# Kernel tuning notes

Measured on AMD Instinct MI355X. Metric: run time of the kernel, lower is better.

The kernel has to match this reference:

```python
import jax, jax.numpy as jnp
import numpy as np

B, T, M, P = 1024, 128, 256, 256  # batch, timesteps, encoder_hidden, decoder_hidden
Tm1 = T - 1


def setup_inputs() -> dict:
    key = jax.random.key(0)
    ks = jax.random.split(key, 10)
    s = lambda k, shape: jax.random.normal(k, shape, jnp.float32) * 0.05
    return {
        "X_encoded": jax.random.normal(ks[0], (B, Tm1, M), jnp.float32),
        "y_prev": jax.random.normal(ks[1], (B, Tm1), jnp.float32),
        # attn_layer: Linear(2P+M -> M), Tanh, Linear(M -> 1)
        "attn_W1": s(ks[2], (M, 2 * P + M)),
        "attn_b1": jnp.zeros((M,), jnp.float32),
        "attn_W2": s(ks[3], (1, M)),
        "attn_b2": jnp.zeros((1,), jnp.float32),
        # LSTM(input_size=1, hidden=P), gate order i,f,g,o
        "W_ih": s(ks[4], (4 * P, 1)),
        "W_hh": s(ks[5], (4 * P, P)),
        "b_ih": jnp.zeros((4 * P,), jnp.float32),
        "b_hh": jnp.zeros((4 * P,), jnp.float32),
        # fc: Linear(M+1 -> 1) (weights init'd normal_() in torch)
        "fc_W": jax.random.normal(ks[6], (1, M + 1), jnp.float32),
        "fc_b": jnp.zeros((1,), jnp.float32),
        # fc_final: Linear(P+M -> 1)
        "fcf_W": s(ks[7], (1, P + M)),
        "fcf_b": jnp.zeros((1,), jnp.float32),
    }


def reference(X_encoded, y_prev, attn_W1, attn_b1, attn_W2, attn_b2,
              W_ih, W_hh, b_ih, b_hh, fc_W, fc_b, fcf_W, fcf_b):
    Bsz, Tsteps, Mdim = X_encoded.shape
    Pdim = W_hh.shape[1]

    def step(carry, y_t):
        d, c, _ = carry  # d,c: [B,P]
        dm = jnp.broadcast_to(d[:, None, :], (Bsz, Tsteps, Pdim))
        cm = jnp.broadcast_to(c[:, None, :], (Bsz, Tsteps, Pdim))
        x = jnp.concatenate([dm, cm, X_encoded], axis=2)  # [B,T-1,2P+M]
        e = jnp.tanh(jnp.einsum('bti,hi->bth', x, attn_W1) + attn_b1)
        scores = jnp.einsum('bth,oh->bto', e, attn_W2)[..., 0] + attn_b2[0]  # [B,T-1]
        beta = jax.nn.softmax(scores, axis=-1)
        context = jnp.einsum('bt,btm->bm', beta, X_encoded)  # [B,M]
        y_tilde = jnp.concatenate([context, y_t[:, None]], axis=1) @ fc_W.T + fc_b  # [B,1]
        gates = y_tilde @ W_ih.T + d @ W_hh.T + (b_ih + b_hh)  # [B,4P]
        i, f, g, o = jnp.split(gates, 4, axis=1)
        c_new = jax.nn.sigmoid(f) * c + jax.nn.sigmoid(i) * jnp.tanh(g)
        d_new = jax.nn.sigmoid(o) * jnp.tanh(c_new)
        return (d_new, c_new, context), None

    init = (jnp.zeros((Bsz, Pdim), X_encoded.dtype),
            jnp.zeros((Bsz, Pdim), X_encoded.dtype),
            jnp.zeros((Bsz, Mdim), X_encoded.dtype))
    (d, c, context), _ = jax.lax.scan(step, init, y_prev.T)  # scan over T-1 steps
    y_pred = jnp.concatenate([d, context], axis=1) @ fcf_W.T + fcf_b  # [B,1]
    return y_pred
```

## Files before the change

kernel.cpp:

```cpp
#include <hip/hip_runtime.h>
#include <hip/hip_bf16.h>

#define TT 127
#define L2E 1.4426950408889634f

typedef __attribute__((ext_vector_type(8))) short s8v;
typedef __attribute__((ext_vector_type(4))) float f4v;

__device__ __forceinline__ float bf2f(unsigned short u){
  union { unsigned int i; float f; } v; v.i = ((unsigned int)u) << 16; return v.f;
}
__device__ __forceinline__ unsigned short f2bf(float f){
  union { float f; unsigned int i; } v; v.f = f;
  unsigned int r = v.i + 0x7FFFu + ((v.i >> 16) & 1u);
  return (unsigned short)(r >> 16);
}
__device__ __forceinline__ float fexp2(float x){ return __builtin_amdgcn_exp2f(x); }
__device__ __forceinline__ float frcp(float x){ return __builtin_amdgcn_rcpf(x); }
__device__ __forceinline__ float sigm(float x){
  return frcp(1.f + fexp2(-L2E * x));
}
__device__ __forceinline__ float tanh_f(float x){
  return 1.f - 2.f * frcp(1.f + fexp2(2.f * L2E * x));
}
__device__ __forceinline__ f4v mfma16(s8v a, s8v b, f4v c){
  return __builtin_amdgcn_mfma_f32_16x16x32_bf16(a, b, c, 0, 0, 0);
}
__device__ __forceinline__ void barrier_lgkm(){
  asm volatile("s_waitcnt lgkmcnt(0)" ::: "memory");
  __builtin_amdgcn_s_barrier();
}

__global__ void k_pack_w1dc(const float* __restrict__ W1, unsigned short* __restrict__ WP){
  int n = blockIdx.x * 256 + threadIdx.x;
  int lane = n & 63, w = (n >> 6) & 15, kt = n >> 10;
  int h = w * 16 + (lane & 15);
  int i0 = kt * 32 + (lane >> 4) * 8;
  #pragma unroll
  for (int j = 0; j < 8; ++j)
    WP[(size_t)n * 8 + j] = f2bf(W1[h * 768 + i0 + j]);
}
__global__ void k_pack_whh(const float* __restrict__ Whh, unsigned short* __restrict__ WP){
  int n = blockIdx.x * 256 + threadIdx.x;
  int lane = n & 63, w = (n >> 6) & 15, f = n >> 10;
  int ct = f >> 3, kt = f & 7;
  int g = (w * 4 + ct) * 16 + (lane & 15);
  int i0 = kt * 32 + (lane >> 4) * 8;
  #pragma unroll
  for (int j = 0; j < 8; ++j)
    WP[131072 + (size_t)n * 8 + j] = f2bf(Whh[g * 256 + i0 + j]);
}

__global__ void k_tr_w1x(const float* __restrict__ W1, float* __restrict__ W1xT){
  int idx = blockIdx.x * 256 + threadIdx.x;
  int k = idx >> 8, h = idx & 255;
  W1xT[idx] = W1[h * 768 + 512 + k];
}

__global__ void k_xfg(const float* __restrict__ X, const float* __restrict__ fcW,
                      const float* __restrict__ fcfW,
                      float* __restrict__ xf, float* __restrict__ xg){
  const int b = blockIdx.x;
  const int w = threadIdx.x >> 6, lane = threadIdx.x & 63;
  f4v wf = *(const f4v*)&fcW[lane * 4];
  f4v wg = *(const f4v*)&fcfW[256 + lane * 4];
  for (int t = w; t < TT; t += 4) {
    f4v x = *(const f4v*)&X[((size_t)b * TT + t) * 256 + lane * 4];
    float af = x[0]*wf[0] + x[1]*wf[1] + x[2]*wf[2] + x[3]*wf[3];
    float ag = x[0]*wg[0] + x[1]*wg[1] + x[2]*wg[2] + x[3]*wg[3];
    #pragma unroll
    for (int m = 32; m; m >>= 1) { af += __shfl_xor(af, m); ag += __shfl_xor(ag, m); }
    if (lane == 0) { xf[(size_t)b * TT + t] = af; xg[(size_t)b * TT + t] = ag; }
  }
}

__global__ __launch_bounds__(256) void k_gemm_tx(
    const float* __restrict__ X, const float* __restrict__ W1xT,
    const float* __restrict__ b1, unsigned short* __restrict__ Tx)
{
  __shared__ float As[16][64];
  __shared__ float Bs[16][64];
  const int row0 = blockIdx.x * 64;
  const int col0 = blockIdx.y * 64;
  const int tid = threadIdx.x;
  const int tx = tid & 15, ty = tid >> 4;
  float acc[4][4] = {};
  for (int k0 = 0; k0 < 256; k0 += 16) {
    {
      const int rr = tid & 63, kk4 = (tid >> 6) << 2;
      float4 v = *(const float4*)&X[(size_t)(row0 + rr) * 256 + k0 + kk4];
      As[kk4 + 0][rr] = v.x; As[kk4 + 1][rr] = v.y;
      As[kk4 + 2][rr] = v.z; As[kk4 + 3][rr] = v.w;
    }
    {
      const int cc = tid & 63, kb = tid >> 6;
      #pragma unroll
      for (int j = 0; j < 4; ++j)
        Bs[kb + 4 * j][cc] = W1xT[(size_t)(k0 + kb + 4 * j) * 256 + col0 + cc];
    }
    __syncthreads();
    #pragma unroll
    for (int kk = 0; kk < 16; ++kk) {
      float4 a4 = *(const float4*)&As[kk][ty << 2];
      float4 b4 = *(const float4*)&Bs[kk][tx << 2];
      float av[4] = {a4.x, a4.y, a4.z, a4.w};
      float bv[4] = {b4.x, b4.y, b4.z, b4.w};
      #pragma unroll
      for (int i = 0; i < 4; ++i)
        #pragma unroll
        for (int j = 0; j < 4; ++j)
          acc[i][j] = fmaf(av[i], bv[j], acc[i][j]);
    }
    __syncthreads();
  }
  const int c = col0 + (tx << 2);
  #pragma unroll
  for (int i = 0; i < 4; ++i) {
    const int r = row0 + (ty << 2) + i;
    ushort4 o;
    o.x = f2bf(tanhf(acc[i][0] + b1[c + 0]));
    o.y = f2bf(tanhf(acc[i][1] + b1[c + 1]));
    o.z = f2bf(tanhf(acc[i][2] + b1[c + 2]));
    o.w = f2bf(tanhf(acc[i][3] + b1[c + 3]));
    *(ushort4*)&Tx[(size_t)r * 256 + c] = o;
  }
}

__global__ __launch_bounds__(1024, 4) void k_main(
    const unsigned short* __restrict__ Tx,
    const unsigned short* __restrict__ WP,
    const float* __restrict__ xf,
    const float* __restrict__ xg,
    const float* __restrict__ yprev,
    const float* __restrict__ W2,
    const float* __restrict__ Wih,
    const float* __restrict__ bih,
    const float* __restrict__ bhh,
    const float* __restrict__ fcW,
    const float* __restrict__ fcb,
    const float* __restrict__ fcfW,
    const float* __restrict__ fcfb,
    float* __restrict__ out)
{
  __shared__ __align__(16) char wring[6 * 16384];
  __shared__ __align__(16) unsigned short dcA[16][520];
  __shared__ __align__(16) float us_s[4][320];
  __shared__ __align__(16) float sc[4][128];
  __shared__ __align__(16) float gts[4][1024];
  __shared__ float w2s[256];
  __shared__ float fcfw_s[256];
  __shared__ float wih_s[1024];
  __shared__ float bsum_s[1024];
  __shared__ float yp_s[4][128];
  __shared__ float xf_s[4][128];
  __shared__ float xg_s[4][128];
  __shared__ float ytil[4];
  __shared__ float sg_s[4];

  const int tid = threadIdx.x;
  const int lane = tid & 63;
  const int w = tid >> 6;
  const int bb = tid >> 8;
  const int hq = tid & 255;
  const int b0 = blockIdx.x << 2;
  const int bq = w >> 2;
  const int cc = lane & 15;
  const int g4 = lane >> 4;

  if (tid < 256) w2s[tid] = W2[tid];
  if (tid >= 256 && tid < 512) fcfw_s[tid - 256] = fcfW[tid - 256];
  wih_s[tid] = Wih[tid];
  bsum_s[tid] = bih[tid] + bhh[tid];
  if (tid < 512 && (tid & 127) < TT)
    yp_s[tid >> 7][tid & 127] = yprev[(size_t)(b0 + (tid >> 7)) * TT + (tid & 127)];
  if (tid >= 512) {
    const int r = (tid - 512) >> 7, c = tid & 127;
    float vf = 0.f, vg = 0.f;
    if (c < TT) {
      vf = xf[(size_t)(b0 + r) * TT + c];
      vg = xg[(size_t)(b0 + r) * TT + c];
    }
    xf_s[r][c] = vf;
    xg_s[r][c] = vg;
  }
  for (int i = tid; i < 16 * 520; i += 1024)
    (&dcA[0][0])[i] = 0;
  const float fcw256 = fcW[256];
  const float fcb0 = fcb[0];
  const float fcfb0 = fcfb[0];
  float creg = 0.f, dreg = 0.f;
  barrier_lgkm();

  const int arow = lane & 15;
  const char* dcbase = (const char*)&dcA[0][0] + arow * 1040 + ((lane >> 4) << 4);
  const int wlo = w * 1024 + lane * 16;
  const char* WPc = (const char*)WP;
  const char* wslice = wring + wlo;
  char* wdst = wring + w * 1024;

  #pragma unroll
  for (int F = 0; F < 6; ++F) {
    __builtin_amdgcn_global_load_lds((const unsigned int*)(WPc + (size_t)F * 16384 + wlo),
                                     (unsigned int*)(wdst + F * 16384), 16, 0, 0);
  }
  asm volatile("s_waitcnt vmcnt(5)" ::: "memory");
  __builtin_amdgcn_sched_barrier(0);
  s8v bnext = *(const s8v*)(wslice);

  for (int t = 0; t < TT; ++t) {
    {
      f4v au0 = {0.f,0.f,0.f,0.f}, au1 = au0;
      f4v ag0 = au0, ag1 = au0, ag2 = au0, ag3 = au0;
      #pragma unroll
      for (int f = 0; f < 48; ++f) {
        s8v bcur = bnext;
        asm volatile("s_waitcnt vmcnt(4)" ::: "memory");
        __builtin_amdgcn_sched_barrier(0);
        bnext = *(const s8v*)(wslice + (((f + 1) % 6) * 16384));
        const int kt = (f < 16) ? f : (f & 7);
        s8v av = *(const s8v*)(dcbase + kt * 64);
        if (f < 16) {
          if (f & 1) au1 = mfma16(av, bcur, au1);
          else       au0 = mfma16(av, bcur, au0);
        } else if (f < 24) {
          ag0 = mfma16(av, bcur, ag0);
        } else if (f < 32) {
          ag1 = mfma16(av, bcur, ag1);
        } else if (f < 40) {
          ag2 = mfma16(av, bcur, ag2);
        } else {
          ag3 = mfma16(av, bcur, ag3);
        }
        const int nf = (f + 6) % 48;
        __builtin_amdgcn_global_load_lds((const unsigned int*)(WPc + (size_t)nf * 16384 + wlo),
                                         (unsigned int*)(wdst + (f % 6) * 16384), 16, 0, 0);
      }
      f4v au = au0 + au1;
      #pragma unroll
      for (int r = 0; r < 4; ++r) {
        au[r] += __shfl_xor(au[r], 16);
        ag0[r] += __shfl_xor(ag0[r], 16);
        ag1[r] += __shfl_xor(ag1[r], 16);
        ag2[r] += __shfl_xor(ag2[r], 16);
        ag3[r] += __shfl_xor(ag3[r], 16);
      }
      if (lane < 16) {
        const int hp = w * 20 + lane;
        #pragma unroll
        for (int r = 0; r < 4; ++r)
          us_s[r][hp] = tanh_f(au[r]);
        #pragma unroll
        for (int r = 0; r < 4; ++r) {
          gts[r][(w * 4 + 0) * 16 + lane] = ag0[r];
          gts[r][(w * 4 + 1) * 16 + lane] = ag1[r];
          gts[r][(w * 4 + 2) * 16 + lane] = ag2[r];
          gts[r][(w * 4 + 3) * 16 + lane] = ag3[r];
        }
      }
    }
    barrier_lgkm();

    {
      float tur[16], w2r[16];
      #pragma unroll
      for (int e4 = 0; e4 < 4; ++e4) {
        f4v tv = *(const f4v*)&us_s[bq][cc * 20 + e4 * 4];
        f4v wv = *(const f4v*)&w2s[cc * 16 + e4 * 4];
        tur[e4*4+0] = tv[0]; tur[e4*4+1] = tv[1]; tur[e4*4+2] = tv[2]; tur[e4*4+3] = tv[3];
        w2r[e4*4+0] = wv[0]; w2r[e4*4+1] = wv[1]; w2r[e4*4+2] = wv[2]; w2r[e4*4+3] = wv[3];
      }
      const unsigned short* txb = &Tx[((size_t)(b0 + bq) * TT) * 256 + cc * 16];
      #pragma unroll
      for (int it = 0; it < 8; ++it) {
        const int tt = it * 16 + (w & 3) * 4 + g4;
        const int ttc = tt < 126 ? tt : 126;
        const unsigned short* p = txb + (size_t)ttc * 256;
        s8v xa = *(const s8v*)p;
        s8v xb = *(const s8v*)(p + 8);
        float a0 = 0.f, a1 = 0.f;
        #pragma unroll
        for (int e = 0; e < 8; ++e) {
          const float x = bf2f((unsigned short)xa[e]);
          a0 = fmaf(w2r[e] * (tur[e] + x), frcp(fmaf(tur[e], x, 1.f)), a0);
        }
        #pragma unroll
        for (int e = 0; e < 8; ++e) {
          const float x = bf2f((unsigned short)xb[e]);
          a1 = fmaf(w2r[8 + e] * (tur[8 + e] + x), frcp(fmaf(tur[8 + e], x, 1.f)), a1);
        }
        float acc = a0 + a1;
        acc += __shfl_xor(acc, 1);
        acc += __shfl_xor(acc, 2);
        acc += __shfl_xor(acc, 4);
        acc += __shfl_xor(acc, 8);
        if (cc == 0 && tt < TT) sc[bq][tt] = acc;
      }
    }
    barrier_lgkm();

    if (w < 4) {
      const float s0 = sc[w][lane];
      const float s1 = (lane < 63) ? sc[w][lane + 64] : -3.0e38f;
      float mx = fmaxf(s0, s1);
      #pragma unroll
      for (int m = 32; m; m >>= 1) mx = fmaxf(mx, __shfl_xor(mx, m));
      const float p0 = fexp2((s0 - mx) * L2E);
      const float p1 = (lane < 63) ? fexp2((s1 - mx) * L2E) : 0.f;
      float sm = p0 + p1;
      float af = fmaf(p0, xf_s[w][lane], p1 * xf_s[w][(lane + 64) & 127]);
      #pragma unroll
      for (int m = 32; m; m >>= 1) {
        sm += __shfl_xor(sm, m);
        af += __shfl_xor(af, m);
      }
      const float inv = frcp(sm);
      if (lane == 0)
        ytil[w] = af * inv + fcw256 * yp_s[w][t] + fcb0;
      if (t == TT - 1) {
        float ag_ = fmaf(p0, xg_s[w][lane], p1 * xg_s[w][(lane + 64) & 127]);
        #pragma unroll
        for (int m = 32; m; m >>= 1) ag_ += __shfl_xor(ag_, m);
        if (lane == 0) sg_s[w] = ag_ * inv;
      }
    }
    barrier_lgkm();

    {
      const float yt = ytil[bb];
      const float gi = gts[bb][hq]       + yt * wih_s[hq]       + bsum_s[hq];
      const float gf = gts[bb][hq + 256] + yt * wih_s[hq + 256] + bsum_s[hq + 256];
      const float gg = gts[bb][hq + 512] + yt * wih_s[hq + 512] + bsum_s[hq + 512];
      const float go = gts[bb][hq + 768] + yt * wih_s[hq + 768] + bsum_s[hq + 768];
      creg = sigm(gf) * creg + sigm(gi) * tanh_f(gg);
      dreg = sigm(go) * tanh_f(creg);
      const unsigned short dh = f2bf(dreg);
      const unsigned short dl = f2bf(dreg - bf2f(dh));
      const unsigned short ch = f2bf(creg);
      const unsigned short cl = f2bf(creg - bf2f(ch));
      dcA[bb][hq] = dh;           dcA[bb + 4][hq] = dl;
      dcA[bb][256 + hq] = ch;     dcA[bb + 4][256 + hq] = cl;
    }
    barrier_lgkm();
  }

  us_s[bb][hq] = dreg;
  barrier_lgkm();
  if (w < 4) {
    float a = 0.f;
    #pragma unroll
    for (int j = 0; j < 4; ++j) {
      const int m = lane + (j << 6);
      a = fmaf(us_s[w][m], fcfw_s[m], a);
    }
    #pragma unroll
    for (int m = 32; m; m >>= 1) a += __shfl_xor(a, m);
    if (lane == 0) out[b0 + w] = a + sg_s[w] + fcfb0;
  }
  asm volatile("s_waitcnt vmcnt(0)" ::: "memory");
}

extern "C" void kernel_launch(void* const* d_in, const int* in_sizes, int n_in,
                              void* d_out, int out_size, void* d_ws, size_t ws_size,
                              hipStream_t stream) {
  const float* X    = (const float*)d_in[0];
  const float* yprev= (const float*)d_in[1];
  const float* W1   = (const float*)d_in[2];
  const float* b1   = (const float*)d_in[3];
  const float* W2   = (const float*)d_in[4];
  const float* Wih  = (const float*)d_in[6];
  const float* Whh  = (const float*)d_in[7];
  const float* bih  = (const float*)d_in[8];
  const float* bhh  = (const float*)d_in[9];
  const float* fcW  = (const float*)d_in[10];
  const float* fcb  = (const float*)d_in[11];
  const float* fcfW = (const float*)d_in[12];
  const float* fcfb = (const float*)d_in[13];
  float* out = (float*)d_out;

  size_t off = 0;
  char* base = (char*)d_ws;
  auto alloc = [&](size_t bytes) -> void* {
    void* p = base + off;
    off += (bytes + 255) & ~(size_t)255;
    return p;
  };
  const size_t txBytes = (size_t)1024 * TT * 256 * 2;
  unsigned short* Tx   = (unsigned short*)alloc(txBytes);
  unsigned short* WP   = (unsigned short*)alloc((size_t)48 * 16384);
  float* W1xT          = (float*)alloc((size_t)256 * 256 * 4);
  float* xf            = (float*)alloc((size_t)1024 * TT * 4);
  float* xg            = (float*)alloc((size_t)1024 * TT * 4);
  (void)in_sizes; (void)n_in; (void)out_size; (void)ws_size;

  k_pack_w1dc<<<64, 256, 0, stream>>>(W1, WP);
  k_pack_whh<<<128, 256, 0, stream>>>(Whh, WP);
  k_tr_w1x<<<256, 256, 0, stream>>>(W1, W1xT);
  k_xfg<<<1024, 256, 0, stream>>>(X, fcW, fcfW, xf, xg);
  dim3 gg(2032, 4);
  k_gemm_tx<<<gg, 256, 0, stream>>>(X, W1xT, b1, Tx);
  k_main<<<256, 1024, 0, stream>>>(Tx, WP, xf, xg, yprev, W2,
                                   Wih, bih, bhh, fcW, fcb, fcfW, fcfb, out);
}
```

Baseline: 4.273 ms.

## Quantize precomputed tanh attention term to int8 and swizzle LDS hidden-state layout

Stores the precomputed tanh(X·W1x+b1) tensor as int8 scaled by 127 instead of bf16. This halves the global-memory traffic the main recurrent kernel re-reads every timestep, and the tanh-addition identity is rewritten to fold the scale into precomputed weights. It also changes the LDS layout of the d/c MFMA operand to an XOR-swizzled padded layout to reduce bank conflicts. The int8 quantization lowers the precision of the attention scores and may affect numerical tolerance.

```diff
diff --git a/kernel.cpp b/kernel.cpp
--- a/kernel.cpp
+++ b/kernel.cpp
@@ -6,6 +6,7 @@
 
 typedef __attribute__((ext_vector_type(8))) short s8v;
 typedef __attribute__((ext_vector_type(4))) float f4v;
+typedef __attribute__((ext_vector_type(4))) int i4v;
 
 __device__ __forceinline__ float bf2f(unsigned short u){
   union { unsigned int i; float f; } v; v.i = ((unsigned int)u) << 16; return v.f;
@@ -76,7 +77,7 @@
 
 __global__ __launch_bounds__(256) void k_gemm_tx(
     const float* __restrict__ X, const float* __restrict__ W1xT,
-    const float* __restrict__ b1, unsigned short* __restrict__ Tx)
+    const float* __restrict__ b1, char* __restrict__ Tx8)
 {
   __shared__ float As[16][64];
   __shared__ float Bs[16][64];
@@ -117,17 +118,17 @@
   #pragma unroll
   for (int i = 0; i < 4; ++i) {
     const int r = row0 + (ty << 2) + i;
-    ushort4 o;
-    o.x = f2bf(tanhf(acc[i][0] + b1[c + 0]));
-    o.y = f2bf(tanhf(acc[i][1] + b1[c + 1]));
-    o.z = f2bf(tanhf(acc[i][2] + b1[c + 2]));
-    o.w = f2bf(tanhf(acc[i][3] + b1[c + 3]));
-    *(ushort4*)&Tx[(size_t)r * 256 + c] = o;
+    uchar4 o;
+    o.x = (unsigned char)(char)rintf(tanhf(acc[i][0] + b1[c + 0]) * 127.f);
+    o.y = (unsigned char)(char)rintf(tanhf(acc[i][1] + b1[c + 1]) * 127.f);
+    o.z = (unsigned char)(char)rintf(tanhf(acc[i][2] + b1[c + 2]) * 127.f);
+    o.w = (unsigned char)(char)rintf(tanhf(acc[i][3] + b1[c + 3]) * 127.f);
+    *(uchar4*)&Tx8[(size_t)r * 256 + c] = o;
   }
 }
 
 __global__ __launch_bounds__(1024, 4) void k_main(
-    const unsigned short* __restrict__ Tx,
+    const char* __restrict__ Tx8,
     const unsigned short* __restrict__ WP,
     const float* __restrict__ xf,
     const float* __restrict__ xg,
@@ -143,7 +144,7 @@
     float* __restrict__ out)
 {
   __shared__ __align__(16) char wring[6 * 16384];
-  __shared__ __align__(16) unsigned short dcA[16][520];
+  __shared__ __align__(16) char dcA8[16 * 1152];
   __shared__ __align__(16) float us_s[4][320];
   __shared__ __align__(16) float sc[4][128];
   __shared__ __align__(16) float gts[4][1024];
@@ -183,8 +184,8 @@
     xf_s[r][c] = vf;
     xg_s[r][c] = vg;
   }
-  for (int i = tid; i < 16 * 520; i += 1024)
-    (&dcA[0][0])[i] = 0;
+  for (int i = tid; i < 16 * 1152 / 2; i += 1024)
+    ((unsigned short*)dcA8)[i] = 0;
   const float fcw256 = fcW[256];
   const float fcb0 = fcb[0];
   const float fcfb0 = fcfb[0];
@@ -192,7 +193,9 @@
   barrier_lgkm();
 
   const int arow = lane & 15;
-  const char* dcbase = (const char*)&dcA[0][0] + arow * 1040 + ((lane >> 4) << 4);
+  const char* arbase = dcA8 + arow * 1152;
+  const int sx4 = (arow & 7) << 4;
+  const int g16 = (lane >> 4) << 4;
   const int wlo = w * 1024 + lane * 16;
   const char* WPc = (const char*)WP;
   const char* wslice = wring + wlo;
@@ -218,7 +221,7 @@
         __builtin_amdgcn_sched_barrier(0);
         bnext = *(const s8v*)(wslice + (((f + 1) % 6) * 16384));
         const int kt = (f < 16) ? f : (f & 7);
-        s8v av = *(const s8v*)(dcbase + kt * 64);
+        s8v av = *(const s8v*)(arbase + ((kt * 64 + g16) ^ sx4));
         if (f < 16) {
           if (f & 1) au1 = mfma16(av, bcur, au1);
           else       au0 = mfma16(av, bcur, au0);
@@ -261,34 +264,38 @@
     barrier_lgkm();
 
     {
-      float tur[16], w2r[16];
+      float tur[16], w2r[16], wt127[16];
       #pragma unroll
       for (int e4 = 0; e4 < 4; ++e4) {
         f4v tv = *(const f4v*)&us_s[bq][cc * 20 + e4 * 4];
         f4v wv = *(const f4v*)&w2s[cc * 16 + e4 * 4];
-        tur[e4*4+0] = tv[0]; tur[e4*4+1] = tv[1]; tur[e4*4+2] = tv[2]; tur[e4*4+3] = tv[3];
-        w2r[e4*4+0] = wv[0]; w2r[e4*4+1] = wv[1]; w2r[e4*4+2] = wv[2]; w2r[e4*4+3] = wv[3];
-      }
-      const unsigned short* txb = &Tx[((size_t)(b0 + bq) * TT) * 256 + cc * 16];
+        #pragma unroll
+        for (int j = 0; j < 4; ++j) {
+          tur[e4*4+j] = tv[j];
+          w2r[e4*4+j] = wv[j];
+          wt127[e4*4+j] = wv[j] * tv[j] * 127.f;
+        }
+      }
+      const char* txb = &Tx8[((size_t)(b0 + bq) * TT) * 256 + cc * 16];
       #pragma unroll
       for (int it = 0; it < 8; ++it) {
         const int tt = it * 16 + (w & 3) * 4 + g4;
         const int ttc = tt < 126 ? tt : 126;
-        const unsigned short* p = txb + (size_t)ttc * 256;
-        s8v xa = *(const s8v*)p;
-        s8v xb = *(const s8v*)(p + 8);
-        float a0 = 0.f, a1 = 0.f;
-        #pragma unroll
-        for (int e = 0; e < 8; ++e) {
-          const float x = bf2f((unsigned short)xa[e]);
-          a0 = fmaf(w2r[e] * (tur[e] + x), frcp(fmaf(tur[e], x, 1.f)), a0);
+        i4v dv = *(const i4v*)(txb + (size_t)ttc * 256);
+        float acc = 0.f;
+        #pragma unroll
+        for (int j = 0; j < 4; ++j) {
+          const int d = dv[j];
+          const float x0 = (float)((d << 24) >> 24);
+          const float x1 = (float)((d << 16) >> 24);
+          const float x2 = (float)((d << 8) >> 24);
+          const float x3 = (float)(d >> 24);
+          const int e = j * 4;
+          acc = fmaf(fmaf(w2r[e+0], x0, wt127[e+0]), frcp(fmaf(tur[e+0], x0, 127.f)), acc);
+          acc = fmaf(fmaf(w2r[e+1], x1, wt127[e+1]), frcp(fmaf(tur[e+1], x1, 127.f)), acc);
+          acc = fmaf(fmaf(w2r[e+2], x2, wt127[e+2]), frcp(fmaf(tur[e+2], x2, 127.f)), acc);
+          acc = fmaf(fmaf(w2r[e+3], x3, wt127[e+3]), frcp(fmaf(tur[e+3], x3, 127.f)), acc);
         }
-        #pragma unroll
-        for (int e = 0; e < 8; ++e) {
-          const float x = bf2f((unsigned short)xb[e]);
-          a1 = fmaf(w2r[8 + e] * (tur[8 + e] + x), frcp(fmaf(tur[8 + e], x, 1.f)), a1);
-        }
-        float acc = a0 + a1;
         acc += __shfl_xor(acc, 1);
         acc += __shfl_xor(acc, 2);
         acc += __shfl_xor(acc, 4);
@@ -337,8 +344,14 @@
       const unsigned short dl = f2bf(dreg - bf2f(dh));
       const unsigned short ch = f2bf(creg);
       const unsigned short cl = f2bf(creg - bf2f(ch));
-      dcA[bb][hq] = dh;           dcA[bb + 4][hq] = dl;
-      dcA[bb][256 + hq] = ch;     dcA[bb + 4][256 + hq] = cl;
+      const int cd = 2 * hq;
+      const int ccol = 512 + 2 * hq;
+      const int sh = (bb & 7) << 4;
+      const int sl = ((bb + 4) & 7) << 4;
+      *(unsigned short*)(dcA8 + bb * 1152       + (((cd & ~15) ^ sh) | (cd & 15)))   = dh;
+      *(unsigned short*)(dcA8 + (bb + 4) * 1152 + (((cd & ~15) ^ sl) | (cd & 15)))   = dl;
+      *(unsigned short*)(dcA8 + bb * 1152       + (((ccol & ~15) ^ sh) | (ccol & 15))) = ch;
+      *(unsigned short*)(dcA8 + (bb + 4) * 1152 + (((ccol & ~15) ^ sl) | (ccol & 15))) = cl;
     }
     barrier_lgkm();
   }
@@ -384,8 +397,7 @@
     off += (bytes + 255) & ~(size_t)255;
     return p;
   };
-  const size_t txBytes = (size_t)1024 * TT * 256 * 2;
-  unsigned short* Tx   = (unsigned short*)alloc(txBytes);
+  char* Tx8            = (char*)alloc((size_t)1024 * TT * 256);
   unsigned short* WP   = (unsigned short*)alloc((size_t)48 * 16384);
   float* W1xT          = (float*)alloc((size_t)256 * 256 * 4);
   float* xf            = (float*)alloc((size_t)1024 * TT * 4);
@@ -397,7 +409,7 @@
   k_tr_w1x<<<256, 256, 0, stream>>>(W1, W1xT);
   k_xfg<<<1024, 256, 0, stream>>>(X, fcW, fcfW, xf, xg);
   dim3 gg(2032, 4);
-  k_gemm_tx<<<gg, 256, 0, stream>>>(X, W1xT, b1, Tx);
-  k_main<<<256, 1024, 0, stream>>>(Tx, WP, xf, xg, yprev, W2,
+  k_gemm_tx<<<gg, 256, 0, stream>>>(X, W1xT, b1, Tx8);
+  k_main<<<256, 1024, 0, stream>>>(Tx8, WP, xf, xg, yprev, W2,
                                    Wih, bih, bhh, fcW, fcb, fcfW, fcfb, out);
 }
```

New measurement: 4.174 ms, median of 2. 2.3% less time.
